# Optimization experiments

Hardware: AMD Instinct MI355X
Metric: run time of the kernel (lower is better)

Reference implementation:

```python
import jax, jax.numpy as jnp
import numpy as np

N_FEAT = 6
EMBED = 256
PAIRS = N_FEAT * (N_FEAT - 1) // 2  # 15
B, S = 32, 512


def setup_inputs() -> dict:
    key = jax.random.key(0)
    k1, k2, k3, k4, k5, k6 = jax.random.split(key, 6)
    features = jax.random.normal(k1, (N_FEAT, B, S, EMBED), dtype=jnp.float32)
    W_pair = jax.random.normal(k2, (PAIRS, 2 * EMBED, EMBED), dtype=jnp.float32) * 0.05
    b_pair = jax.random.normal(k3, (PAIRS, EMBED), dtype=jnp.float32) * 0.05
    W_final = jax.random.normal(k4, (PAIRS * EMBED, EMBED), dtype=jnp.float32) * 0.02
    b_final = jax.random.normal(k5, (EMBED,), dtype=jnp.float32) * 0.02
    NAS = jax.random.randint(k6, (N_FEAT,), 0, 2, dtype=jnp.int32)
    return {"features": features, "W_pair": W_pair, "b_pair": b_pair,
            "W_final": W_final, "b_final": b_final, "NAS": NAS}


def reference(features, W_pair, b_pair, W_final, b_final, NAS):
    n = features.shape[0]
    # static pair index order matches the nested loops: (0,1),(0,2),...,(n-2,n-1)
    i_idx, j_idx = np.triu_indices(n, k=1)
    nas = NAS.at[:2].set(1)  # encoder_input=True forces first two features on
    pair_mask = (nas[i_idx] * nas[j_idx]).astype(features.dtype)  # [P]
    # pairwise concat + linear + tanh, batched over all P pairs
    xcat = jnp.concatenate([features[i_idx], features[j_idx]], axis=-1)  # [P,B,S,2D]
    h = jnp.tanh(jnp.einsum('pbsk,pkd->pbsd', xcat, W_pair) + b_pair[:, None, None, :])
    h = h * pair_mask[:, None, None, None]  # zero out inactive pairs (ZeroNormal)
    P, Bb, Ss, D = h.shape
    # concat along last dim in pair order, then final linear
    flat = jnp.transpose(h, (1, 2, 0, 3)).reshape(Bb, Ss, P * D)  # [B,S,P*D]
    return flat @ W_final + b_final
```

## Files before the change

### kernel.cpp

```cpp
#include <hip/hip_runtime.h>
#include <hip/hip_bf16.h>


typedef unsigned short u16;
typedef __bf16 bf16x8 __attribute__((ext_vector_type(8)));
typedef float f32x4 __attribute__((ext_vector_type(4)));

#define BS 16384
#define EMB 256
#define PAIRS 15
#define XRS 40

__constant__ int c_pi[PAIRS] = {0,0,0,0,0,1,1,1,1,2,2,2,3,3,4};
__constant__ int c_pj[PAIRS] = {1,2,3,4,5,2,3,4,5,3,4,5,4,5,5};

__device__ __forceinline__ u16 f2bf_u(float x) {
    __bf16 b = (__bf16)x;
    return __builtin_bit_cast(u16, b);
}

__global__ __launch_bounds__(256) void transpose_cvt2(
    const float* __restrict__ Wp, const float* __restrict__ Wf,
    u16* __restrict__ Wp_t, u16* __restrict__ Wf_t)
{
    __shared__ float t[32][33];
    const int z = blockIdx.z;
    const float* in;
    u16* out;
    int R;
    if (z < PAIRS) { R = 512;  in = Wp + (size_t)z * 512 * 256; out = Wp_t + (size_t)z * 256 * 512; }
    else           { R = 3840; in = Wf;                          out = Wf_t; }
    const int r0 = blockIdx.x * 32;
    if (r0 >= R) return;
    const int c0 = blockIdx.y * 32;
    const int tr = threadIdx.x >> 5;
    const int tc = threadIdx.x & 31;
#pragma unroll
    for (int pass = 0; pass < 4; ++pass)
        t[pass * 8 + tr][tc] = in[(size_t)(r0 + pass * 8 + tr) * 256 + c0 + tc];
    __syncthreads();
#pragma unroll
    for (int pass = 0; pass < 4; ++pass)
        out[(size_t)(c0 + pass * 8 + tr) * R + r0 + tc] = f2bf_u(t[tc][pass * 8 + tr]);
}


__device__ __forceinline__ void stage_tile(const u16* gsrc, int row_stride_us,
                                           int col_off_us, u16* lds_base, int tid) {
    int wave = tid >> 6;
#pragma unroll
    for (int r = 0; r < 2; ++r) {
        int c  = r * 512 + tid;
        int n  = c & 255;
        int kb = c >> 8;
        const u16* g = gsrc + (size_t)n * row_stride_us + col_off_us + kb * 8;
        u16* l = lds_base + (size_t)(r * 512 + wave * 64) * 8;
        __builtin_amdgcn_global_load_lds(
            (const __attribute__((address_space(1))) void*)g,
            (__attribute__((address_space(3))) void*)l,
            16, 0, 0);
    }
}

__device__ __forceinline__ void stage_x(const float* fsrc, int t0, int col0,
                                        u16* ldsx, int tid) {
    const int row = tid >> 3;
    const int cg  = (tid & 7) * 4;
    f32x4 v = *(const f32x4*)(fsrc + (size_t)(t0 + row) * EMB + col0 + cg);
    ushort4 o;
    o.x = f2bf_u(v[0]); o.y = f2bf_u(v[1]); o.z = f2bf_u(v[2]); o.w = f2bf_u(v[3]);
    *(ushort4*)(ldsx + row * XRS + cg) = o;
}

__global__ __launch_bounds__(512, 4) void fused_cblock(
    const float* __restrict__ feats,
    const u16* __restrict__ Wp_t,
    const float* __restrict__ b_pair,
    const u16* __restrict__ Wf_t,
    const float* __restrict__ b_final,
    const int* __restrict__ NAS,
    float* __restrict__ out)
{
    __shared__ u16 lds_b[2][8192];
    __shared__ u16 lds_h[64 * 264];
    __shared__ u16 lds_x[2][64 * XRS];

    const int tid  = threadIdx.x;
    const int lane = tid & 63;
    const int wave = tid >> 6;
    const int wm   = wave & 1;
    const int wn   = wave >> 1;
    const int quad = lane >> 4;
    const int l16  = lane & 15;
    const int t0   = blockIdx.x * 64;

    stage_tile(Wp_t, 512, 0, lds_b[0], tid);
    stage_x(feats , t0, 0, lds_x[0], tid);

    const f32x4 fzero = {0.f, 0.f, 0.f, 0.f};
    f32x4 acc2[8];
#pragma unroll
    for (int i = 0; i < 8; ++i) acc2[i] = fzero;

    int nasv[6];
#pragma unroll
    for (int f = 0; f < 6; ++f) nasv[f] = (f < 2) ? 1 : (NAS[f] != 0 ? 1 : 0);
    int pmask = 0;
#pragma unroll
    for (int p = 0; p < PAIRS; ++p)
        if (nasv[c_pi[p]] & nasv[c_pj[p]]) pmask |= (1 << p);

    __syncthreads();

    for (int p = 0; p < PAIRS; ++p) {
        if (!((pmask >> p) & 1)) continue;
        const int fi = c_pi[p], fj = c_pj[p];
        const u16* WpT = Wp_t + (size_t)p * 256 * 512;
        const int rest  = pmask >> (p + 1);
        const int pnext = rest ? (p + 1 + __builtin_ctz(rest)) : -1;

        f32x4 acc1[8];
#pragma unroll
        for (int i = 0; i < 8; ++i) acc1[i] = fzero;

        for (int ks = 0; ks < 16; ++ks) {
            const int cur = ks & 1;
            if (ks < 15) {
                stage_tile(WpT, 512, (ks + 1) * 32, lds_b[1 - cur], tid);
                stage_x(feats + (size_t)((ks + 1 < 8) ? fi : fj) * BS * EMB,
                        t0, ((ks + 1) & 7) * 32, lds_x[1 - cur], tid);
            } else {
                stage_tile(Wf_t, 3840, p * 256, lds_b[1 - cur], tid);
            }
            bf16x8 a0 = *(const bf16x8*)(&lds_x[cur][(wm * 32 + l16) * XRS + quad * 8]);
            bf16x8 a1 = *(const bf16x8*)(&lds_x[cur][(wm * 32 + 16 + l16) * XRS + quad * 8]);
#pragma unroll
            for (int nt = 0; nt < 4; ++nt) {
                const int n = wn * 64 + nt * 16 + l16;
                bf16x8 b = *(const bf16x8*)(&lds_b[cur][(quad * 256 + n) * 8]);
                acc1[nt]     = __builtin_amdgcn_mfma_f32_16x16x32_bf16(a0, b, acc1[nt],     0, 0, 0);
                acc1[4 + nt] = __builtin_amdgcn_mfma_f32_16x16x32_bf16(a1, b, acc1[4 + nt], 0, 0, 0);
            }
            __syncthreads();
        }

#pragma unroll
        for (int mt = 0; mt < 2; ++mt)
#pragma unroll
        for (int nt = 0; nt < 4; ++nt) {
            const int n = wn * 64 + nt * 16 + l16;
            const float bias = b_pair[p * 256 + n];
#pragma unroll
            for (int r = 0; r < 4; ++r) {
                const int row = wm * 32 + mt * 16 + quad * 4 + r;
                lds_h[row * 264 + n] = f2bf_u(tanhf(acc1[mt * 4 + nt][r] + bias));
            }
        }
        __syncthreads();

        for (int ks = 0; ks < 8; ++ks) {
            const int cur = ks & 1;
            if (ks < 7)
                stage_tile(Wf_t, 3840, p * 256 + (ks + 1) * 32, lds_b[1 - cur], tid);
            else if (pnext >= 0)
                stage_tile(Wp_t + (size_t)pnext * 256 * 512, 512, 0, lds_b[1 - cur], tid);
            if (ks == 0 && pnext >= 0)
                stage_x(feats + (size_t)c_pi[pnext] * BS * EMB, t0, 0, lds_x[0], tid);
            const int e0 = ks * 32 + quad * 8;
            bf16x8 a0 = *(const bf16x8*)(&lds_h[(wm * 32 + l16) * 264 + e0]);
            bf16x8 a1 = *(const bf16x8*)(&lds_h[(wm * 32 + 16 + l16) * 264 + e0]);
#pragma unroll
            for (int nt = 0; nt < 4; ++nt) {
                const int n = wn * 64 + nt * 16 + l16;
                bf16x8 b = *(const bf16x8*)(&lds_b[cur][(quad * 256 + n) * 8]);
                acc2[nt]     = __builtin_amdgcn_mfma_f32_16x16x32_bf16(a0, b, acc2[nt],     0, 0, 0);
                acc2[4 + nt] = __builtin_amdgcn_mfma_f32_16x16x32_bf16(a1, b, acc2[4 + nt], 0, 0, 0);
            }
            __syncthreads();
        }
    }

#pragma unroll
    for (int mt = 0; mt < 2; ++mt)
#pragma unroll
    for (int nt = 0; nt < 4; ++nt) {
        const int n = wn * 64 + nt * 16 + l16;
        const float bf = b_final[n];
#pragma unroll
        for (int r = 0; r < 4; ++r) {
            const int t = t0 + wm * 32 + mt * 16 + quad * 4 + r;
            out[(size_t)t * EMB + n] = acc2[mt * 4 + nt][r] + bf;
        }
    }
}


#define TOK 4

__global__ __launch_bounds__(256) void fallback_cblock(
    const float* __restrict__ feats, const float* __restrict__ W_pair,
    const float* __restrict__ b_pair, const float* __restrict__ W_final,
    const float* __restrict__ b_final, const int* __restrict__ NAS,
    float* __restrict__ out)
{
    __shared__ float xs[TOK][6 * 256];
    __shared__ float hf[TOK][PAIRS * 256];

    const int n  = threadIdx.x;
    const int t0 = blockIdx.x * TOK;

#pragma unroll
    for (int tk = 0; tk < TOK; ++tk)
#pragma unroll
        for (int f = 0; f < 6; ++f)
            xs[tk][f * 256 + n] = feats[((size_t)f * BS + t0 + tk) * EMB + n];
    __syncthreads();

    int nasv[6];
#pragma unroll
    for (int f = 0; f < 6; ++f) nasv[f] = (f < 2) ? 1 : (NAS[f] != 0 ? 1 : 0);

    for (int p = 0; p < PAIRS; ++p) {
        const int fi = c_pi[p], fj = c_pj[p];
        if (!(nasv[fi] & nasv[fj])) {
#pragma unroll
            for (int tk = 0; tk < TOK; ++tk) hf[tk][p * 256 + n] = 0.f;
            continue;
        }
        float acc[TOK];
        const float bias = b_pair[p * 256 + n];
#pragma unroll
        for (int tk = 0; tk < TOK; ++tk) acc[tk] = bias;
        const float* Wp = W_pair + (size_t)p * 512 * 256;
#pragma unroll 4
        for (int k = 0; k < 512; ++k) {
            const float w = Wp[(size_t)k * 256 + n];
            const int xoff = ((k < 256) ? fi : fj) * 256 + (k & 255);
#pragma unroll
            for (int tk = 0; tk < TOK; ++tk) acc[tk] += xs[tk][xoff] * w;
        }
#pragma unroll
        for (int tk = 0; tk < TOK; ++tk)
            hf[tk][p * 256 + n] = tanhf(acc[tk]);
    }
    __syncthreads();

    float acc[TOK];
    const float bf = b_final[n];
#pragma unroll
    for (int tk = 0; tk < TOK; ++tk) acc[tk] = bf;
#pragma unroll 4
    for (int k = 0; k < PAIRS * 256; ++k) {
        const float w = W_final[(size_t)k * 256 + n];
#pragma unroll
        for (int tk = 0; tk < TOK; ++tk) acc[tk] += hf[tk][k] * w;
    }
#pragma unroll
    for (int tk = 0; tk < TOK; ++tk)
        out[(size_t)(t0 + tk) * EMB + n] = acc[tk];
}


extern "C" void kernel_launch(void* const* d_in, const int* in_sizes, int n_in,
                              void* d_out, int out_size, void* d_ws, size_t ws_size,
                              hipStream_t stream) {
    const float* feats   = (const float*)d_in[0];
    const float* W_pair  = (const float*)d_in[1];
    const float* b_pair  = (const float*)d_in[2];
    const float* W_final = (const float*)d_in[3];
    const float* b_final = (const float*)d_in[4];
    const int*   NAS     = (const int*)d_in[5];

    const size_t needed = ((size_t)PAIRS * 256 * 512 + (size_t)256 * 3840) * 2;

    if (ws_size >= needed) {
        u16* Wp_t = (u16*)d_ws;
        u16* Wf_t = Wp_t + (size_t)PAIRS * 256 * 512;
        transpose_cvt2<<<dim3(3840 / 32, 256 / 32, PAIRS + 1), 256, 0, stream>>>(
            W_pair, W_final, Wp_t, Wf_t);
        fused_cblock<<<BS / 64, 512, 0, stream>>>(feats, Wp_t, b_pair, Wf_t,
                                                  b_final, NAS, (float*)d_out);
    } else {
        fallback_cblock<<<BS / TOK, 256, 0, stream>>>(feats, W_pair, b_pair,
                                                      W_final, b_final, NAS,
                                                      (float*)d_out);
    }
}
```

Measured before the change: 179.5 us.

## Triple-buffer weight tiles with prefetch depth two and custom vmcnt barriers

Moves the weight tile staging from double to triple buffering, so async global-to-LDS loads run two k-steps ahead, and replaces __syncthreads with a barrier that waits only until vmcnt drops to 2. The feature load is issued before the MFMAs and converted to LDS afterwards to hide its latency, and pair biases are preloaded into LDS. The extra LDS forces launch bounds from 4 to 2 blocks per CU, which lowers occupancy. The partial vmcnt wait also depends on exact load counting to stay correct.

```diff
diff --git a/kernel.cpp b/kernel.cpp
--- a/kernel.cpp
+++ b/kernel.cpp
@@ -62,17 +62,14 @@
     }
 }
 
-__device__ __forceinline__ void stage_x(const float* fsrc, int t0, int col0,
-                                        u16* ldsx, int tid) {
-    const int row = tid >> 3;
-    const int cg  = (tid & 7) * 4;
-    f32x4 v = *(const f32x4*)(fsrc + (size_t)(t0 + row) * EMB + col0 + cg);
-    ushort4 o;
-    o.x = f2bf_u(v[0]); o.y = f2bf_u(v[1]); o.z = f2bf_u(v[2]); o.w = f2bf_u(v[3]);
-    *(ushort4*)(ldsx + row * XRS + cg) = o;
-}
-
-__global__ __launch_bounds__(512, 4) void fused_cblock(
+__device__ __forceinline__ void phase_barrier() {
+    asm volatile("s_waitcnt vmcnt(2) lgkmcnt(0)" ::: "memory");
+    __builtin_amdgcn_sched_barrier(0);
+    __builtin_amdgcn_s_barrier();
+    __builtin_amdgcn_sched_barrier(0);
+}
+
+__global__ __launch_bounds__(512, 2) void fused_cblock(
     const float* __restrict__ feats,
     const u16* __restrict__ Wp_t,
     const float* __restrict__ b_pair,
@@ -81,9 +78,10 @@
     const int* __restrict__ NAS,
     float* __restrict__ out)
 {
-    __shared__ u16 lds_b[2][8192];
-    __shared__ u16 lds_h[64 * 264];
-    __shared__ u16 lds_x[2][64 * XRS];
+    __shared__ u16   lds_b[3][8192];
+    __shared__ u16   lds_h[64 * 264];
+    __shared__ u16   lds_x[2][64 * XRS];
+    __shared__ float lds_bias[PAIRS * 256];
 
     const int tid  = threadIdx.x;
     const int lane = tid & 63;
@@ -93,24 +91,44 @@
     const int quad = lane >> 4;
     const int l16  = lane & 15;
     const int t0   = blockIdx.x * 64;
-
-    stage_tile(Wp_t, 512, 0, lds_b[0], tid);
-    stage_x(feats , t0, 0, lds_x[0], tid);
+    const int xrow = tid >> 3;
+    const int xcg  = (tid & 7) * 4;
+
+    int nasv[6];
+#pragma unroll
+    for (int f = 0; f < 6; ++f) nasv[f] = (f < 2) ? 1 : (NAS[f] != 0 ? 1 : 0);
+    int pmask = 0;
+#pragma unroll
+    for (int p = 0; p < PAIRS; ++p)
+        if (nasv[c_pi[p]] & nasv[c_pj[p]]) pmask |= (1 << p);
+
+    float btmp[8];
+#pragma unroll
+    for (int i = 0; i < 8; ++i) {
+        const int idx = tid + i * 512;
+        btmp[i] = (idx < PAIRS * 256) ? b_pair[idx] : 0.f;
+    }
+#pragma unroll
+    for (int i = 0; i < 8; ++i) {
+        const int idx = tid + i * 512;
+        if (idx < PAIRS * 256) lds_bias[idx] = btmp[i];
+    }
+    f32x4 xv = *(const f32x4*)(feats + (size_t)(t0 + xrow) * EMB + xcg);
+    stage_tile(Wp_t, 512, 0,  lds_b[0], tid);
+    stage_tile(Wp_t, 512, 32, lds_b[1], tid);
+    {
+        ushort4 o;
+        o.x = f2bf_u(xv[0]); o.y = f2bf_u(xv[1]);
+        o.z = f2bf_u(xv[2]); o.w = f2bf_u(xv[3]);
+        *(ushort4*)(&lds_x[0][xrow * XRS + xcg]) = o;
+    }
 
     const f32x4 fzero = {0.f, 0.f, 0.f, 0.f};
     f32x4 acc2[8];
 #pragma unroll
     for (int i = 0; i < 8; ++i) acc2[i] = fzero;
 
-    int nasv[6];
-#pragma unroll
-    for (int f = 0; f < 6; ++f) nasv[f] = (f < 2) ? 1 : (NAS[f] != 0 ? 1 : 0);
-    int pmask = 0;
-#pragma unroll
-    for (int p = 0; p < PAIRS; ++p)
-        if (nasv[c_pi[p]] & nasv[c_pj[p]]) pmask |= (1 << p);
-
-    __syncthreads();
+    int bcur = 0, bw = 2;
 
     for (int p = 0; p < PAIRS; ++p) {
         if (!((pmask >> p) & 1)) continue;
@@ -124,61 +142,92 @@
         for (int i = 0; i < 8; ++i) acc1[i] = fzero;
 
         for (int ks = 0; ks < 16; ++ks) {
-            const int cur = ks & 1;
-            if (ks < 15) {
-                stage_tile(WpT, 512, (ks + 1) * 32, lds_b[1 - cur], tid);
-                stage_x(feats + (size_t)((ks + 1 < 8) ? fi : fj) * BS * EMB,
-                        t0, ((ks + 1) & 7) * 32, lds_x[1 - cur], tid);
+            phase_barrier();
+            const int sl = ks + 1;
+            const float* xsrc;
+            int xcol;
+            if (sl < 16) {
+                xsrc = feats + (size_t)((sl < 8) ? fi : fj) * BS * EMB;
+                xcol = (sl & 7) * 32;
             } else {
-                stage_tile(Wf_t, 3840, p * 256, lds_b[1 - cur], tid);
-            }
-            bf16x8 a0 = *(const bf16x8*)(&lds_x[cur][(wm * 32 + l16) * XRS + quad * 8]);
-            bf16x8 a1 = *(const bf16x8*)(&lds_x[cur][(wm * 32 + 16 + l16) * XRS + quad * 8]);
+                const int nf = (pnext >= 0) ? c_pi[pnext] : fi;
+                xsrc = feats + (size_t)nf * BS * EMB;
+                xcol = 0;
+            }
+            f32x4 v = *(const f32x4*)(xsrc + (size_t)(t0 + xrow) * EMB + xcol + xcg);
+            __builtin_amdgcn_sched_barrier(0);
+            {
+                const u16* gp; int rs, co;
+                const int idx = ks + 2;
+                if (idx <= 15)      { gp = WpT;  rs = 512;  co = idx * 32; }
+                else if (idx == 16) { gp = Wf_t; rs = 3840; co = p * 256; }
+                else                { gp = Wf_t; rs = 3840; co = p * 256 + 32; }
+                stage_tile(gp, rs, co, lds_b[bw], tid);
+            }
+            __builtin_amdgcn_sched_barrier(0);
+            bf16x8 a0 = *(const bf16x8*)(&lds_x[ks & 1][(wm * 32 + l16) * XRS + quad * 8]);
+            bf16x8 a1 = *(const bf16x8*)(&lds_x[ks & 1][(wm * 32 + 16 + l16) * XRS + quad * 8]);
 #pragma unroll
             for (int nt = 0; nt < 4; ++nt) {
                 const int n = wn * 64 + nt * 16 + l16;
-                bf16x8 b = *(const bf16x8*)(&lds_b[cur][(quad * 256 + n) * 8]);
+                bf16x8 b = *(const bf16x8*)(&lds_b[bcur][(quad * 256 + n) * 8]);
                 acc1[nt]     = __builtin_amdgcn_mfma_f32_16x16x32_bf16(a0, b, acc1[nt],     0, 0, 0);
                 acc1[4 + nt] = __builtin_amdgcn_mfma_f32_16x16x32_bf16(a1, b, acc1[4 + nt], 0, 0, 0);
             }
-            __syncthreads();
-        }
-
-#pragma unroll
-        for (int mt = 0; mt < 2; ++mt)
+            __builtin_amdgcn_sched_barrier(0);
+            {
+                ushort4 o;
+                o.x = f2bf_u(v[0]); o.y = f2bf_u(v[1]);
+                o.z = f2bf_u(v[2]); o.w = f2bf_u(v[3]);
+                *(ushort4*)(&lds_x[sl & 1][xrow * XRS + xcg]) = o;
+            }
+            bcur = (bcur == 2) ? 0 : bcur + 1;
+            bw   = (bw   == 2) ? 0 : bw   + 1;
+        }
+
 #pragma unroll
         for (int nt = 0; nt < 4; ++nt) {
             const int n = wn * 64 + nt * 16 + l16;
-            const float bias = b_pair[p * 256 + n];
+            const float bias = lds_bias[p * 256 + n];
+#pragma unroll
+            for (int mt = 0; mt < 2; ++mt)
 #pragma unroll
             for (int r = 0; r < 4; ++r) {
                 const int row = wm * 32 + mt * 16 + quad * 4 + r;
                 lds_h[row * 264 + n] = f2bf_u(tanhf(acc1[mt * 4 + nt][r] + bias));
             }
         }
-        __syncthreads();
 
         for (int ks = 0; ks < 8; ++ks) {
-            const int cur = ks & 1;
-            if (ks < 7)
-                stage_tile(Wf_t, 3840, p * 256 + (ks + 1) * 32, lds_b[1 - cur], tid);
-            else if (pnext >= 0)
-                stage_tile(Wp_t + (size_t)pnext * 256 * 512, 512, 0, lds_b[1 - cur], tid);
-            if (ks == 0 && pnext >= 0)
-                stage_x(feats + (size_t)c_pi[pnext] * BS * EMB, t0, 0, lds_x[0], tid);
+            phase_barrier();
+            {
+                const u16* gp; int rs, co;
+                const int idx = ks + 2;
+                if (idx <= 7) { gp = Wf_t; rs = 3840; co = p * 256 + idx * 32; }
+                else {
+                    const int np = (pnext >= 0) ? pnext : p;
+                    gp = Wp_t + (size_t)np * 256 * 512; rs = 512; co = (idx - 8) * 32;
+                }
+                stage_tile(gp, rs, co, lds_b[bw], tid);
+            }
+            __builtin_amdgcn_sched_barrier(0);
             const int e0 = ks * 32 + quad * 8;
             bf16x8 a0 = *(const bf16x8*)(&lds_h[(wm * 32 + l16) * 264 + e0]);
             bf16x8 a1 = *(const bf16x8*)(&lds_h[(wm * 32 + 16 + l16) * 264 + e0]);
 #pragma unroll
             for (int nt = 0; nt < 4; ++nt) {
                 const int n = wn * 64 + nt * 16 + l16;
-                bf16x8 b = *(const bf16x8*)(&lds_b[cur][(quad * 256 + n) * 8]);
+                bf16x8 b = *(const bf16x8*)(&lds_b[bcur][(quad * 256 + n) * 8]);
                 acc2[nt]     = __builtin_amdgcn_mfma_f32_16x16x32_bf16(a0, b, acc2[nt],     0, 0, 0);
                 acc2[4 + nt] = __builtin_amdgcn_mfma_f32_16x16x32_bf16(a1, b, acc2[4 + nt], 0, 0, 0);
             }
-            __syncthreads();
-        }
-    }
+            __builtin_amdgcn_sched_barrier(0);
+            bcur = (bcur == 2) ? 0 : bcur + 1;
+            bw   = (bw   == 2) ? 0 : bw   + 1;
+        }
+    }
+
+    asm volatile("s_waitcnt vmcnt(0)" ::: "memory");
 
 #pragma unroll
     for (int mt = 0; mt < 2; ++mt)
```

New measurement: 178.9 us. Within noise of the previous version (-0.3%).

## Stage full feature panels in LDS via register prefetch instead of per-k-step slices

Applied to the files above, without the earlier changes.

Replaces the per-k-step staging of 32-column feature slices with whole 64x256 feature panels held in LDS. Each panel is loaded into registers early in the loop and written to LDS after the MFMA work of the eighth step, so global load latency overlaps compute and fewer tiny loads are issued per step. The cost is much more LDS (three 64x264 buffers) and 32 extra registers per thread. Launch bounds drop from 4 to 2 blocks per SM, which lowers occupancy.

```diff
diff --git a/kernel.cpp b/kernel.cpp
--- a/kernel.cpp
+++ b/kernel.cpp
@@ -9,7 +9,7 @@
 #define BS 16384
 #define EMB 256
 #define PAIRS 15
-#define XRS 40
+#define XR 264
 
 __constant__ int c_pi[PAIRS] = {0,0,0,0,0,1,1,1,1,2,2,2,3,3,4};
 __constant__ int c_pj[PAIRS] = {1,2,3,4,5,2,3,4,5,3,4,5,4,5,5};
@@ -62,17 +62,25 @@
     }
 }
 
-__device__ __forceinline__ void stage_x(const float* fsrc, int t0, int col0,
-                                        u16* ldsx, int tid) {
-    const int row = tid >> 3;
-    const int cg  = (tid & 7) * 4;
-    f32x4 v = *(const f32x4*)(fsrc + (size_t)(t0 + row) * EMB + col0 + cg);
-    ushort4 o;
-    o.x = f2bf_u(v[0]); o.y = f2bf_u(v[1]); o.z = f2bf_u(v[2]); o.w = f2bf_u(v[3]);
-    *(ushort4*)(ldsx + row * XRS + cg) = o;
-}
-
-__global__ __launch_bounds__(512, 4) void fused_cblock(
+__device__ __forceinline__ void xpanel_load(const float* fsrc, int t0,
+                                            int xrow, int xcg, f32x4* xb) {
+#pragma unroll
+    for (int i = 0; i < 8; ++i)
+        xb[i] = *(const f32x4*)(fsrc + (size_t)(t0 + xrow) * EMB + i * 32 + xcg);
+}
+
+__device__ __forceinline__ void xpanel_write(const f32x4* xb, u16* ldsx,
+                                             int xrow, int xcg) {
+#pragma unroll
+    for (int i = 0; i < 8; ++i) {
+        ushort4 o;
+        o.x = f2bf_u(xb[i][0]); o.y = f2bf_u(xb[i][1]);
+        o.z = f2bf_u(xb[i][2]); o.w = f2bf_u(xb[i][3]);
+        *(ushort4*)(&ldsx[xrow * XR + i * 32 + xcg]) = o;
+    }
+}
+
+__global__ __launch_bounds__(512, 2) void fused_cblock(
     const float* __restrict__ feats,
     const u16* __restrict__ Wp_t,
     const float* __restrict__ b_pair,
@@ -82,8 +90,9 @@
     float* __restrict__ out)
 {
     __shared__ u16 lds_b[2][8192];
-    __shared__ u16 lds_h[64 * 264];
-    __shared__ u16 lds_x[2][64 * XRS];
+    __shared__ u16 lds_xA[64 * XR];
+    __shared__ u16 lds_xB[64 * XR];
+    __shared__ u16 lds_h[64 * XR];
 
     const int tid  = threadIdx.x;
     const int lane = tid & 63;
@@ -93,28 +102,31 @@
     const int quad = lane >> 4;
     const int l16  = lane & 15;
     const int t0   = blockIdx.x * 64;
-
+    const int xrow = tid >> 3;
+    const int xcg  = (tid & 7) * 4;
+
+    int nasv[6];
+#pragma unroll
+    for (int f = 0; f < 6; ++f) nasv[f] = (f < 2) ? 1 : (NAS[f] != 0 ? 1 : 0);
+    int pmask = 0;
+#pragma unroll
+    for (int p = 0; p < PAIRS; ++p)
+        if (nasv[c_pi[p]] & nasv[c_pj[p]]) pmask |= (1 << p);
+
+    f32x4 xb[8];
+    xpanel_load(feats, t0, xrow, xcg, xb);
     stage_tile(Wp_t, 512, 0, lds_b[0], tid);
-    stage_x(feats , t0, 0, lds_x[0], tid);
+    xpanel_write(xb, lds_xA, xrow, xcg);
+    __syncthreads();
 
     const f32x4 fzero = {0.f, 0.f, 0.f, 0.f};
     f32x4 acc2[8];
 #pragma unroll
     for (int i = 0; i < 8; ++i) acc2[i] = fzero;
 
-    int nasv[6];
-#pragma unroll
-    for (int f = 0; f < 6; ++f) nasv[f] = (f < 2) ? 1 : (NAS[f] != 0 ? 1 : 0);
-    int pmask = 0;
-#pragma unroll
-    for (int p = 0; p < PAIRS; ++p)
-        if (nasv[c_pi[p]] & nasv[c_pj[p]]) pmask |= (1 << p);
-
-    __syncthreads();
-
     for (int p = 0; p < PAIRS; ++p) {
         if (!((pmask >> p) & 1)) continue;
-        const int fi = c_pi[p], fj = c_pj[p];
+        const int fj = c_pj[p];
         const u16* WpT = Wp_t + (size_t)p * 256 * 512;
         const int rest  = pmask >> (p + 1);
         const int pnext = rest ? (p + 1 + __builtin_ctz(rest)) : -1;
@@ -125,15 +137,16 @@
 
         for (int ks = 0; ks < 16; ++ks) {
             const int cur = ks & 1;
-            if (ks < 15) {
+            if (ks == 0)
+                xpanel_load(feats + (size_t)fj * BS * EMB, t0, xrow, xcg, xb);
+            if (ks < 15)
                 stage_tile(WpT, 512, (ks + 1) * 32, lds_b[1 - cur], tid);
-                stage_x(feats + (size_t)((ks + 1 < 8) ? fi : fj) * BS * EMB,
-                        t0, ((ks + 1) & 7) * 32, lds_x[1 - cur], tid);
-            } else {
+            else
                 stage_tile(Wf_t, 3840, p * 256, lds_b[1 - cur], tid);
-            }
-            bf16x8 a0 = *(const bf16x8*)(&lds_x[cur][(wm * 32 + l16) * XRS + quad * 8]);
-            bf16x8 a1 = *(const bf16x8*)(&lds_x[cur][(wm * 32 + 16 + l16) * XRS + quad * 8]);
+            const u16* xs = (ks < 8) ? lds_xA : lds_xB;
+            const int ko = (ks & 7) * 32 + quad * 8;
+            bf16x8 a0 = *(const bf16x8*)(&xs[(wm * 32 + l16) * XR + ko]);
+            bf16x8 a1 = *(const bf16x8*)(&xs[(wm * 32 + 16 + l16) * XR + ko]);
 #pragma unroll
             for (int nt = 0; nt < 4; ++nt) {
                 const int n = wn * 64 + nt * 16 + l16;
@@ -141,6 +154,8 @@
                 acc1[nt]     = __builtin_amdgcn_mfma_f32_16x16x32_bf16(a0, b, acc1[nt],     0, 0, 0);
                 acc1[4 + nt] = __builtin_amdgcn_mfma_f32_16x16x32_bf16(a1, b, acc1[4 + nt], 0, 0, 0);
             }
+            if (ks == 7)
+                xpanel_write(xb, lds_xB, xrow, xcg);
             __syncthreads();
         }
 
@@ -153,22 +168,23 @@
 #pragma unroll
             for (int r = 0; r < 4; ++r) {
                 const int row = wm * 32 + mt * 16 + quad * 4 + r;
-                lds_h[row * 264 + n] = f2bf_u(tanhf(acc1[mt * 4 + nt][r] + bias));
+                lds_h[row * XR + n] = f2bf_u(tanhf(acc1[mt * 4 + nt][r] + bias));
             }
         }
         __syncthreads();
 
         for (int ks = 0; ks < 8; ++ks) {
             const int cur = ks & 1;
+            if (ks == 0 && pnext >= 0)
+                xpanel_load(feats + (size_t)c_pi[pnext] * BS * EMB, t0, xrow, xcg, xb);
             if (ks < 7)
                 stage_tile(Wf_t, 3840, p * 256 + (ks + 1) * 32, lds_b[1 - cur], tid);
-            else if (pnext >= 0)
-                stage_tile(Wp_t + (size_t)pnext * 256 * 512, 512, 0, lds_b[1 - cur], tid);
-            if (ks == 0 && pnext >= 0)
-                stage_x(feats + (size_t)c_pi[pnext] * BS * EMB, t0, 0, lds_x[0], tid);
+            else
+                stage_tile(Wp_t + (size_t)((pnext >= 0) ? pnext : p) * 256 * 512,
+                           512, 0, lds_b[1 - cur], tid);
             const int e0 = ks * 32 + quad * 8;
-            bf16x8 a0 = *(const bf16x8*)(&lds_h[(wm * 32 + l16) * 264 + e0]);
-            bf16x8 a1 = *(const bf16x8*)(&lds_h[(wm * 32 + 16 + l16) * 264 + e0]);
+            bf16x8 a0 = *(const bf16x8*)(&lds_h[(wm * 32 + l16) * XR + e0]);
+            bf16x8 a1 = *(const bf16x8*)(&lds_h[(wm * 32 + 16 + l16) * XR + e0]);
 #pragma unroll
             for (int nt = 0; nt < 4; ++nt) {
                 const int n = wn * 64 + nt * 16 + l16;
@@ -176,6 +192,8 @@
                 acc2[nt]     = __builtin_amdgcn_mfma_f32_16x16x32_bf16(a0, b, acc2[nt],     0, 0, 0);
                 acc2[4 + nt] = __builtin_amdgcn_mfma_f32_16x16x32_bf16(a1, b, acc2[4 + nt], 0, 0, 0);
             }
+            if (ks == 7 && pnext >= 0)
+                xpanel_write(xb, lds_xA, xrow, xcg);
             __syncthreads();
         }
     }
```

New measurement: 179.8 us. No clear change (+0.2%).
